# Performance work log

Measured on AMD Instinct MI355X. Metric: run time of the kernel, lower is better.

## Reference

```python
import jax, jax.numpy as jnp
import numpy as np

N, E, C, R, HID = 50000, 500000, 64, 16, 64


def setup_inputs() -> dict:
    key = jax.random.key(0)
    ks = jax.random.split(key, 24)
    g = lambda k, shape, s=1.0: jax.random.normal(k, shape, dtype=jnp.float32) * s
    cs = C ** -0.5
    inp = {
        "h": g(ks[0], (N, 4 * C)),                                  # [N, 64x0e | 64x1o]
        "edge_index": jax.random.randint(ks[1], (2, E), 0, N),       # row0 = sender, row1 = receiver
        "edge_sh": g(ks[2], (E, 4)),                                 # Y_00, Y_1m (1x0e+1x1o)
        "edge_rbf": g(ks[3], (E, R)),                                # radial embedding 16x0e
        # interaction: linear_up (per-l channel mixing)
        "W_up0": g(ks[4], (C, C), cs), "W_up1": g(ks[5], (C, C), cs),
        # radial MLP 16->64->64->64->4*C (4 uvu tensor-product paths per channel)
        "M1": g(ks[6], (R, HID), R ** -0.5), "M2": g(ks[7], (HID, HID), HID ** -0.5),
        "M3": g(ks[8], (HID, HID), HID ** -0.5), "M4": g(ks[9], (HID, 4 * C), HID ** -0.5),
        # post-scatter linear
        "W_lin0": g(ks[10], (C, C), cs), "W_lin1": g(ks[11], (C, C), cs),
        # skip tensor product with 1x0e node attrs == linear residual
        "Wsc0": g(ks[12], (C, C), cs), "Wsc1": g(ks[13], (C, C), cs),
        # symmetric contraction weights (correlation <=3): 0e paths [a, a^2, v.v, a^3, a*v.v], 1o paths [v, a*v, a^2*v, (v.v)*v]
        "Wc0": g(ks[14], (C, 5)), "Wc1": g(ks[15], (C, 4)),
        # product-basis output linear
        "WB0": g(ks[16], (C, C), cs), "WB1": g(ks[17], (C, C), cs),
        # equivariant batchnorm affine params
        "gamma0": jnp.ones((C,), jnp.float32), "beta0": jnp.zeros((C,), jnp.float32),
        "gamma1": jnp.ones((C,), jnp.float32),
    }
    return inp


def reference(h, edge_index, edge_sh, edge_rbf, W_up0, W_up1, M1, M2, M3, M4,
              W_lin0, W_lin1, Wsc0, Wsc1, Wc0, Wc1, WB0, WB1, gamma0, beta0, gamma1):
    n = h.shape[0]
    h0 = h[:, :C]                        # [N,C] scalars
    h1 = h[:, C:].reshape(n, C, 3)       # [N,C,3] vectors

    # ---- interaction: linear_up ----
    up0 = h0 @ W_up0
    up1 = jnp.einsum('ncx,cd->ndx', h1, W_up1)

    # ---- radial MLP -> per-edge tensor-product weights [E,4,C] ----
    r = jax.nn.silu(edge_rbf @ M1)
    r = jax.nn.silu(r @ M2)
    r = jax.nn.silu(r @ M3)
    tpw = (r @ M4).reshape(-1, 4, C)

    # ---- gather + channelwise (uvu) tensor product with edge sh ----
    snd, rcv = edge_index[0], edge_index[1]
    x0 = up0[snd]                        # [E,C]
    x1 = up1[snd]                        # [E,C,3]
    sh0 = edge_sh[:, 0]                  # [E]
    sh1 = edge_sh[:, 1:]                 # [E,3]
    inv3 = 1.0 / jnp.sqrt(jnp.float32(3.0))
    # paths: 0e*0e->0e, 0e*1o->1o, 1o*0e->1o, 1o*1o->0e (dot)
    m0e = tpw[:, 0] * x0 * sh0[:, None] + tpw[:, 3] * jnp.einsum('ecx,ex->ec', x1, sh1) * inv3
    m1e = (tpw[:, 1][:, :, None] * x0[:, :, None] * sh1[:, None, :]
           + tpw[:, 2][:, :, None] * x1 * sh0[:, None, None])

    # ---- scatter-sum to receivers (avg_num_neighbors = 1.0) ----
    msg0 = jax.ops.segment_sum(m0e, rcv, num_segments=n)
    msg1 = jax.ops.segment_sum(m1e, rcv, num_segments=n)

    # ---- post linear -> A features; skip connection sc ----
    A0 = msg0 @ W_lin0
    A1 = jnp.einsum('ncx,cd->ndx', msg1, W_lin1)
    sc0 = h0 @ Wsc0
    sc1 = jnp.einsum('ncx,cd->ndx', h1, Wsc1)

    # ---- product basis: symmetric contraction up to correlation 3 ----
    vv = jnp.sum(A1 * A1, -1)            # [N,C]
    B0 = (Wc0[:, 0] * A0 + Wc0[:, 1] * A0 * A0 + Wc0[:, 2] * vv
          + Wc0[:, 3] * A0 ** 3 + Wc0[:, 4] * A0 * vv)
    B1 = (Wc1[:, 0] + Wc1[:, 1] * A0 + Wc1[:, 2] * A0 * A0 + Wc1[:, 3] * vv)[..., None] * A1
    o0 = B0 @ WB0 + sc0
    o1 = jnp.einsum('ncx,cd->ndx', B1, WB1) + sc1

    # ---- equivariant batchnorm: mean/var for 0e, norm-only for 1o ----
    eps = jnp.float32(1e-5)
    mu = jnp.mean(o0, 0)
    xc = o0 - mu
    var = jnp.mean(xc * xc, 0)
    n0 = xc * jax.lax.rsqrt(var + eps) * gamma0 + beta0
    nrm1 = jnp.mean(jnp.sum(o1 * o1, -1) / 3.0, 0)
    n1 = o1 * (jax.lax.rsqrt(nrm1 + eps) * gamma1)[None, :, None]

    return jnp.concatenate([n0, n1.reshape(n, 3 * C)], -1)
```

## Files before the change

kernel.cpp:

```cpp
#include <hip/hip_runtime.h>
#include <hip/hip_fp16.h>
#include <math.h>

#define NN 50000
#define NE 500000

typedef __attribute__((ext_vector_type(8))) short bf16x8;
typedef __attribute__((ext_vector_type(4))) float f32x4;

__device__ __forceinline__ float silu_f(float x) {
  return x / (1.0f + __expf(-x));
}
__device__ __forceinline__ unsigned short f2bf(float x) {
  union { float f; unsigned u; } v;
  v.f = x;
  unsigned r = v.u + 0x7fffu + ((v.u >> 16) & 1u);
  return (unsigned short)(r >> 16);
}
__device__ __forceinline__ unsigned short f2h(float x) {
  __half h = __float2half(x);
  return *reinterpret_cast<unsigned short*>(&h);
}
__device__ __forceinline__ float h2f(unsigned short u) {
  __half h = *reinterpret_cast<__half*>(&u);
  return __half2float(h);
}
__device__ __forceinline__ void splitbf(float x, unsigned short& hi_,
                                        unsigned short& lo_) {
  unsigned short h = f2bf(x);
  union { unsigned u; float f; } v;
  v.u = (unsigned)h << 16;
  hi_ = h;
  lo_ = f2bf(x - v.f);
}
__device__ __forceinline__ int swz64(int row, int col) {
  return row * 64 + ((((col >> 3) ^ (row & 7)) << 3) | (col & 7));
}
__device__ __forceinline__ int swz32(int row, int col) {
  return row * 32 + ((((col >> 3) ^ (row & 3)) << 3) | (col & 7));
}
__device__ __forceinline__ bf16x8 wfrag(const unsigned short* Wt, int n,
                                        int kc, int q) {
  return *reinterpret_cast<const bf16x8*>(
      &Wt[n * 64 + (((kc * 4 + q) ^ (n & 7)) << 3)]);
}
__device__ __forceinline__ bf16x8 ldfrag(const float* p) {
  float4 f0 = *reinterpret_cast<const float4*>(p);
  float4 f1 = *reinterpret_cast<const float4*>(p + 4);
  bf16x8 a;
  a[0] = (short)f2bf(f0.x); a[1] = (short)f2bf(f0.y);
  a[2] = (short)f2bf(f0.z); a[3] = (short)f2bf(f0.w);
  a[4] = (short)f2bf(f1.x); a[5] = (short)f2bf(f1.y);
  a[6] = (short)f2bf(f1.z); a[7] = (short)f2bf(f1.w);
  return a;
}
__device__ __forceinline__ void ldfrag2(const float* p, bf16x8& hi,
                                        bf16x8& lo) {
  float4 f0 = *reinterpret_cast<const float4*>(p);
  float4 f1 = *reinterpret_cast<const float4*>(p + 4);
  float a[8] = {f0.x, f0.y, f0.z, f0.w, f1.x, f1.y, f1.z, f1.w};
#pragma unroll
  for (int i = 0; i < 8; ++i) {
    unsigned short h, l2;
    splitbf(a[i], h, l2);
    hi[i] = (short)h;
    lo[i] = (short)l2;
  }
}
__device__ __forceinline__ f32x4 mfma_(bf16x8 a, bf16x8 b, f32x4 cacc) {
  return __builtin_amdgcn_mfma_f32_16x16x32_bf16(a, b, cacc, 0, 0, 0);
}

__global__ __launch_bounds__(256) void ksort1(const int* __restrict__ eidx,
                                              int* __restrict__ hist) {
  int e = blockIdx.x * 256 + threadIdx.x;
  if (e < NE) atomicAdd(&hist[eidx[NE + e]], 1);
}

__global__ __launch_bounds__(1024) void ksort2(const int* __restrict__ hist,
                                               int* __restrict__ cursor) {
  __shared__ int bs[1024];
  const int t = threadIdx.x;
  const int CH = (NN + 1023) / 1024;
  const int lo = t * CH, hi = (lo + CH < NN) ? lo + CH : NN;
  int s = 0;
  for (int i = lo; i < hi; ++i) s += hist[i];
  bs[t] = s;
  __syncthreads();
  for (int off = 1; off < 1024; off <<= 1) {
    int v = (t >= off) ? bs[t - off] : 0;
    __syncthreads();
    bs[t] += v;
    __syncthreads();
  }
  int run = bs[t] - s;
  for (int i = lo; i < hi; ++i) {
    cursor[i] = run;
    run += hist[i];
  }
}

__global__ __launch_bounds__(256) void ksort3(const int* __restrict__ eidx,
                                              int* __restrict__ cursor,
                                              int* __restrict__ perm) {
  int e = blockIdx.x * 256 + threadIdx.x;
  if (e < NE) {
    int p = atomicAdd(&cursor[eidx[NE + e]], 1);
    perm[p] = e;
  }
}

__global__ __launch_bounds__(256) void kup(
    const float* __restrict__ h, const float* __restrict__ Wup0,
    const float* __restrict__ Wup1, unsigned short* __restrict__ upb) {
  __shared__ float shd[4][256];
  const int w = threadIdx.x >> 6, j = threadIdx.x & 63;
  const int n = blockIdx.x * 4 + w;
  const float* hr = h + (size_t)n * 256;
#pragma unroll
  for (int t = 0; t < 4; ++t) shd[w][t * 64 + j] = hr[t * 64 + j];
  __syncthreads();
  float a0 = 0.f, ax = 0.f, ay = 0.f, az = 0.f;
#pragma unroll 8
  for (int c = 0; c < 64; ++c) {
    float h0 = shd[w][c];
    float hx = shd[w][64 + 3 * c + 0];
    float hy = shd[w][64 + 3 * c + 1];
    float hz = shd[w][64 + 3 * c + 2];
    float w0 = Wup0[c * 64 + j];
    float w1 = Wup1[c * 64 + j];
    a0 = fmaf(h0, w0, a0);
    ax = fmaf(hx, w1, ax);
    ay = fmaf(hy, w1, ay);
    az = fmaf(hz, w1, az);
  }
  ushort4 pk;
  pk.x = f2h(a0);
  pk.y = f2h(ax);
  pk.z = f2h(ay);
  pk.w = f2h(az);
  *reinterpret_cast<ushort4*>(upb + ((size_t)n * 64 + j) * 4) = pk;
}

__global__ __launch_bounds__(512) void kedge(
    const float* __restrict__ rbf, const int* __restrict__ eidx,
    const float* __restrict__ esh, const float* __restrict__ M1,
    const float* __restrict__ M2, const float* __restrict__ M3,
    const float* __restrict__ M4, const unsigned short* __restrict__ upb,
    const int* __restrict__ perm, float* __restrict__ msg0,
    float* __restrict__ msg1) {
  __shared__ unsigned short M1t[64 * 32];
  __shared__ unsigned short M2t[64 * 64];
  __shared__ unsigned short M3t[64 * 64];
  __shared__ unsigned short M4t[256 * 64];
  __shared__ unsigned short actS[8][32 * 64];
  const int tid = threadIdx.x;
  const int w = tid >> 6, l = tid & 63;
  const int c = l & 15, q = l >> 4;

  for (int i = tid; i < 2048; i += 512) {
    int o = i >> 5, k = i & 31;
    M1t[swz32(o, k)] = (k < 16) ? f2bf(M1[k * 64 + o]) : (unsigned short)0;
  }
  for (int i = tid; i < 4096; i += 512) {
    int k = i >> 6, o = i & 63;
    M2t[swz64(o, k)] = f2bf(M2[i]);
    M3t[swz64(o, k)] = f2bf(M3[i]);
  }
  for (int i = tid; i < 16384; i += 512) {
    int k = i >> 8, o = i & 255;
    M4t[swz64(o, k)] = f2bf(M4[i]);
  }
  __syncthreads();

  unsigned short* act = actS[w];
  const float inv3 = 0.57735026918962576f;
  const int NW = NE / 32;
  const int scq = (c >> 2) * 8 + (c & 3);

  for (int grp = blockIdx.x; grp < (NW + 7) / 8; grp += gridDim.x) {
    const int gw = grp * 8 + w;
    if (gw >= NW) continue;
    const int eb = gw * 32;

#pragma unroll
    for (int t = 0; t < 2; ++t) {
      const int sc = scq + t * 4;
      bf16x8 a1 = {};
      if (q < 2) {
        const int pec = perm[eb + sc];
        const float* p = rbf + (size_t)pec * 16 + q * 8;
        float4 f0 = *reinterpret_cast<const float4*>(p);
        float4 f1 = *reinterpret_cast<const float4*>(p + 4);
        a1[0] = (short)f2bf(f0.x); a1[1] = (short)f2bf(f0.y);
        a1[2] = (short)f2bf(f0.z); a1[3] = (short)f2bf(f0.w);
        a1[4] = (short)f2bf(f1.x); a1[5] = (short)f2bf(f1.y);
        a1[6] = (short)f2bf(f1.z); a1[7] = (short)f2bf(f1.w);
      }
      f32x4 acc[4];
#pragma unroll
      for (int nt = 0; nt < 4; ++nt) {
        int n = nt * 16 + c;
        bf16x8 b = *reinterpret_cast<const bf16x8*>(&M1t[n * 32 + ((q ^ (n & 3)) << 3)]);
        f32x4 z = {0.f, 0.f, 0.f, 0.f};
        acc[nt] = __builtin_amdgcn_mfma_f32_16x16x32_bf16(a1, b, z, 0, 0, 0);
      }
#pragma unroll
      for (int nt = 0; nt < 4; ++nt)
#pragma unroll
        for (int r = 0; r < 4; ++r)
          act[swz64(q * 8 + t * 4 + r, nt * 16 + c)] = f2bf(silu_f(acc[nt][r]));

      {
        bf16x8 a0 = *reinterpret_cast<const bf16x8*>(&act[sc * 64 + (((0 + q) ^ (sc & 7)) << 3)]);
        bf16x8 a1b = *reinterpret_cast<const bf16x8*>(&act[sc * 64 + (((4 + q) ^ (sc & 7)) << 3)]);
#pragma unroll
        for (int nt = 0; nt < 4; ++nt) {
          int n = nt * 16 + c;
          f32x4 z = {0.f, 0.f, 0.f, 0.f};
          acc[nt] = __builtin_amdgcn_mfma_f32_16x16x32_bf16(a0, wfrag(M2t, n, 0, q), z, 0, 0, 0);
          acc[nt] = __builtin_amdgcn_mfma_f32_16x16x32_bf16(a1b, wfrag(M2t, n, 1, q), acc[nt], 0, 0, 0);
        }
#pragma unroll
        for (int nt = 0; nt < 4; ++nt)
#pragma unroll
          for (int r = 0; r < 4; ++r)
            act[swz64(q * 8 + t * 4 + r, nt * 16 + c)] = f2bf(silu_f(acc[nt][r]));
      }
      {
        bf16x8 a0 = *reinterpret_cast<const bf16x8*>(&act[sc * 64 + (((0 + q) ^ (sc & 7)) << 3)]);
        bf16x8 a1b = *reinterpret_cast<const bf16x8*>(&act[sc * 64 + (((4 + q) ^ (sc & 7)) << 3)]);
#pragma unroll
        for (int nt = 0; nt < 4; ++nt) {
          int n = nt * 16 + c;
          f32x4 z = {0.f, 0.f, 0.f, 0.f};
          acc[nt] = __builtin_amdgcn_mfma_f32_16x16x32_bf16(a0, wfrag(M3t, n, 0, q), z, 0, 0, 0);
          acc[nt] = __builtin_amdgcn_mfma_f32_16x16x32_bf16(a1b, wfrag(M3t, n, 1, q), acc[nt], 0, 0, 0);
        }
#pragma unroll
        for (int nt = 0; nt < 4; ++nt)
#pragma unroll
          for (int r = 0; r < 4; ++r)
            act[swz64(q * 8 + t * 4 + r, nt * 16 + c)] = f2bf(silu_f(acc[nt][r]));
      }
    }

    int sn[8], rvv[8];
    float4 shv[8];
#pragma unroll
    for (int r8 = 0; r8 < 8; ++r8) {
      const int e2 = perm[eb + 8 * q + r8];
      sn[r8] = eidx[e2];
      rvv[r8] = eidx[NE + e2];
      shv[r8] = *reinterpret_cast<const float4*>(esh + (size_t)e2 * 4);
    }
    bf16x8 a0t[2], a1t[2];
#pragma unroll
    for (int t = 0; t < 2; ++t) {
      const int sc = scq + t * 4;
      a0t[t] = *reinterpret_cast<const bf16x8*>(&act[sc * 64 + (((0 + q) ^ (sc & 7)) << 3)]);
      a1t[t] = *reinterpret_cast<const bf16x8*>(&act[sc * 64 + (((4 + q) ^ (sc & 7)) << 3)]);
    }
#pragma unroll
    for (int j2 = 0; j2 < 4; ++j2) {
      const int ch = j2 * 16 + c;
      float acc0 = 0.f, accx = 0.f, accy = 0.f, accz = 0.f;
      int cur = rvv[0];
#pragma unroll
      for (int t = 0; t < 2; ++t) {
        ushort4 xv[4];
#pragma unroll
        for (int r = 0; r < 4; ++r)
          xv[r] = *reinterpret_cast<const ushort4*>(
              upb + ((size_t)sn[4 * t + r] * 64 + ch) * 4);
        f32x4 t4[4];
#pragma unroll
        for (int m = 0; m < 4; ++m) {
          int n = (m * 4 + j2) * 16 + c;
          f32x4 z = {0.f, 0.f, 0.f, 0.f};
          t4[m] = __builtin_amdgcn_mfma_f32_16x16x32_bf16(a0t[t], wfrag(M4t, n, 0, q), z, 0, 0, 0);
          t4[m] = __builtin_amdgcn_mfma_f32_16x16x32_bf16(a1t[t], wfrag(M4t, n, 1, q), t4[m], 0, 0, 0);
        }
#pragma unroll
        for (int r = 0; r < 4; ++r) {
          const int idx = 4 * t + r;
          float x0 = h2f(xv[r].x);
          float xx = h2f(xv[r].y);
          float xy = h2f(xv[r].z);
          float xz = h2f(xv[r].w);
          float t0v = t4[0][r], t1v = t4[1][r];
          float t2v = t4[2][r], t3v = t4[3][r];
          float4 sh4 = shv[idx];
          float dot = xx * sh4.y + xy * sh4.z + xz * sh4.w;
          float m0 = t0v * x0 * sh4.x + t3v * dot * inv3;
          float a1v = t1v * x0, b1v = t2v * sh4.x;
          float m1x = fmaf(a1v, sh4.y, b1v * xx);
          float m1y = fmaf(a1v, sh4.z, b1v * xy);
          float m1z = fmaf(a1v, sh4.w, b1v * xz);
          if (rvv[idx] != cur) {
            atomicAdd(msg0 + (size_t)cur * 64 + ch, acc0);
            atomicAdd(msg1 + (size_t)cur * 192 + ch, accx);
            atomicAdd(msg1 + (size_t)cur * 192 + 64 + ch, accy);
            atomicAdd(msg1 + (size_t)cur * 192 + 128 + ch, accz);
            cur = rvv[idx];
            acc0 = accx = accy = accz = 0.f;
          }
          acc0 += m0;
          accx += m1x;
          accy += m1y;
          accz += m1z;
        }
      }
      atomicAdd(msg0 + (size_t)cur * 64 + ch, acc0);
      atomicAdd(msg1 + (size_t)cur * 192 + ch, accx);
      atomicAdd(msg1 + (size_t)cur * 192 + 64 + ch, accy);
      atomicAdd(msg1 + (size_t)cur * 192 + 128 + ch, accz);
    }
  }
}

__global__ __launch_bounds__(512) void knode(
    const float* __restrict__ msg0, const float* __restrict__ msg1,
    const float* __restrict__ h, const float* __restrict__ Wl0,
    const float* __restrict__ Wl1, const float* __restrict__ Wsc0,
    const float* __restrict__ Wsc1, const float* __restrict__ Wc0,
    const float* __restrict__ Wc1, const float* __restrict__ WB0,
    const float* __restrict__ WB1, float* __restrict__ out,
    float* __restrict__ stat) {
  extern __shared__ unsigned short klds[];
  unsigned short* actS = klds + 10 * 4096;
  const int tid = threadIdx.x, w = tid >> 6, l = tid & 63;
  const int c = l & 15, q = l >> 4;
  for (int i = tid; i < 4096; i += 512) {
    int k = i >> 6, o = i & 63;
    int s = swz64(o, k);
    unsigned short hi, lo;
    splitbf(Wl0[i], hi, lo);
    klds[s] = hi; klds[4096 + s] = lo;
    splitbf(Wl1[i], hi, lo);
    klds[2 * 4096 + s] = hi; klds[3 * 4096 + s] = lo;
    klds[4 * 4096 + s] = f2bf(Wsc0[i]);
    klds[5 * 4096 + s] = f2bf(Wsc1[i]);
    splitbf(WB0[i], hi, lo);
    klds[6 * 4096 + s] = hi; klds[7 * 4096 + s] = lo;
    splitbf(WB1[i], hi, lo);
    klds[8 * 4096 + s] = hi; klds[9 * 4096 + s] = lo;
  }
  __syncthreads();
  const int gw = blockIdx.x * 8 + w;
  const bool valid = (gw < NN / 16);
  const int gws = valid ? gw : 0;
  const int n0 = gws * 16;
  const int nc = n0 + c;
  unsigned short* actH = actS + w * 2048;
  unsigned short* actL = actH + 1024;
  const unsigned short* Wl0h = klds;
  const unsigned short* Wl0l = klds + 4096;
  const unsigned short* Wl1h = klds + 2 * 4096;
  const unsigned short* Wl1l = klds + 3 * 4096;
  const unsigned short* Wsc0t = klds + 4 * 4096;
  const unsigned short* Wsc1t = klds + 5 * 4096;
  const unsigned short* WB0h = klds + 6 * 4096;
  const unsigned short* WB0l = klds + 7 * 4096;
  const unsigned short* WB1h = klds + 8 * 4096;
  const unsigned short* WB1l = klds + 9 * 4096;

  f32x4 aA0[4], aA1[3][4];
  {
    bf16x8 h0, l0, h1, l1;
    ldfrag2(msg0 + (size_t)nc * 64 + q * 8, h0, l0);
    ldfrag2(msg0 + (size_t)nc * 64 + 32 + q * 8, h1, l1);
#pragma unroll
    for (int nt = 0; nt < 4; ++nt) {
      int n = nt * 16 + c;
      f32x4 z = {0.f, 0.f, 0.f, 0.f};
      f32x4 v = mfma_(h0, wfrag(Wl0h, n, 0, q), z);
      v = mfma_(l0, wfrag(Wl0h, n, 0, q), v);
      v = mfma_(h0, wfrag(Wl0l, n, 0, q), v);
      v = mfma_(h1, wfrag(Wl0h, n, 1, q), v);
      v = mfma_(l1, wfrag(Wl0h, n, 1, q), v);
      v = mfma_(h1, wfrag(Wl0l, n, 1, q), v);
      aA0[nt] = v;
    }
#pragma unroll
    for (int x = 0; x < 3; ++x) {
      ldfrag2(msg1 + (size_t)nc * 192 + x * 64 + q * 8, h0, l0);
      ldfrag2(msg1 + (size_t)nc * 192 + x * 64 + 32 + q * 8, h1, l1);
#pragma unroll
      for (int nt = 0; nt < 4; ++nt) {
        int n = nt * 16 + c;
        f32x4 z = {0.f, 0.f, 0.f, 0.f};
        f32x4 v = mfma_(h0, wfrag(Wl1h, n, 0, q), z);
        v = mfma_(l0, wfrag(Wl1h, n, 0, q), v);
        v = mfma_(h0, wfrag(Wl1l, n, 0, q), v);
        v = mfma_(h1, wfrag(Wl1h, n, 1, q), v);
        v = mfma_(l1, wfrag(Wl1h, n, 1, q), v);
        v = mfma_(h1, wfrag(Wl1l, n, 1, q), v);
        aA1[x][nt] = v;
      }
    }
  }
#pragma unroll
  for (int nt = 0; nt < 4; ++nt) {
    const int ch = nt * 16 + c;
    const float* wc0 = Wc0 + ch * 5;
    const float4 c1 = *reinterpret_cast<const float4*>(Wc1 + ch * 4);
#pragma unroll
    for (int r = 0; r < 4; ++r) {
      float A0v = aA0[nt][r];
      float ax = aA1[0][nt][r], ay = aA1[1][nt][r], az = aA1[2][nt][r];
      float vv = ax * ax + ay * ay + az * az;
      float A02 = A0v * A0v;
      float B0 = wc0[0] * A0v + wc0[1] * A02 + wc0[2] * vv +
                 wc0[3] * A02 * A0v + wc0[4] * A0v * vv;
      float sB = c1.x + c1.y * A0v + c1.z * A02 + c1.w * vv;
      aA0[nt][r] = B0;
      aA1[0][nt][r] = sB * ax;
      aA1[1][nt][r] = sB * ay;
      aA1[2][nt][r] = sB * az;
    }
  }
  float st0[4], sq0[4], st1[4];
#pragma unroll
  for (int nt = 0; nt < 4; ++nt) { st0[nt] = 0.f; sq0[nt] = 0.f; st1[nt] = 0.f; }
  const float* hrow = h + (size_t)nc * 256;

  {
#pragma unroll
    for (int nt = 0; nt < 4; ++nt)
#pragma unroll
      for (int r = 0; r < 4; ++r) {
        unsigned short hh, ll;
        splitbf(aA0[nt][r], hh, ll);
        int s = swz64(4 * q + r, nt * 16 + c);
        actH[s] = hh;
        actL[s] = ll;
      }
    __syncthreads();
    bf16x8 bh0 = *reinterpret_cast<const bf16x8*>(&actH[c * 64 + ((q ^ (c & 7)) << 3)]);
    bf16x8 bh1 = *reinterpret_cast<const bf16x8*>(&actH[c * 64 + (((4 + q) ^ (c & 7)) << 3)]);
    bf16x8 bl0 = *reinterpret_cast<const bf16x8*>(&actL[c * 64 + ((q ^ (c & 7)) << 3)]);
    bf16x8 bl1 = *reinterpret_cast<const bf16x8*>(&actL[c * 64 + (((4 + q) ^ (c & 7)) << 3)]);
    __syncthreads();
    bf16x8 ah0 = ldfrag(hrow + q * 8);
    bf16x8 ah1 = ldfrag(hrow + 32 + q * 8);
    f32x4 o[4];
#pragma unroll
    for (int nt = 0; nt < 4; ++nt) {
      int n = nt * 16 + c;
      f32x4 z = {0.f, 0.f, 0.f, 0.f};
      f32x4 v = mfma_(ah0, wfrag(Wsc0t, n, 0, q), z);
      v = mfma_(ah1, wfrag(Wsc0t, n, 1, q), v);
      v = mfma_(bh0, wfrag(WB0h, n, 0, q), v);
      v = mfma_(bh1, wfrag(WB0h, n, 1, q), v);
      v = mfma_(bl0, wfrag(WB0h, n, 0, q), v);
      v = mfma_(bl1, wfrag(WB0h, n, 1, q), v);
      v = mfma_(bh0, wfrag(WB0l, n, 0, q), v);
      v = mfma_(bh1, wfrag(WB0l, n, 1, q), v);
      o[nt] = v;
    }
    if (valid) {
#pragma unroll
      for (int nt = 0; nt < 4; ++nt) {
        const int ch = nt * 16 + c;
#pragma unroll
        for (int r = 0; r < 4; ++r) {
          float v = o[nt][r];
          out[(size_t)(n0 + 4 * q + r) * 256 + ch] = v;
          st0[nt] += v;
          sq0[nt] = fmaf(v, v, sq0[nt]);
        }
      }
    }
  }
#pragma unroll
  for (int x = 0; x < 3; ++x) {
#pragma unroll
    for (int nt = 0; nt < 4; ++nt)
#pragma unroll
      for (int r = 0; r < 4; ++r) {
        unsigned short hh, ll;
        splitbf(aA1[x][nt][r], hh, ll);
        int s = swz64(4 * q + r, nt * 16 + c);
        actH[s] = hh;
        actL[s] = ll;
      }
    __syncthreads();
    bf16x8 bh0 = *reinterpret_cast<const bf16x8*>(&actH[c * 64 + ((q ^ (c & 7)) << 3)]);
    bf16x8 bh1 = *reinterpret_cast<const bf16x8*>(&actH[c * 64 + (((4 + q) ^ (c & 7)) << 3)]);
    bf16x8 bl0 = *reinterpret_cast<const bf16x8*>(&actL[c * 64 + ((q ^ (c & 7)) << 3)]);
    bf16x8 bl1 = *reinterpret_cast<const bf16x8*>(&actL[c * 64 + (((4 + q) ^ (c & 7)) << 3)]);
    __syncthreads();
    bf16x8 ah0, ah1;
#pragma unroll
    for (int i = 0; i < 8; ++i) {
      ah0[i] = (short)f2bf(hrow[64 + (q * 8 + i) * 3 + x]);
      ah1[i] = (short)f2bf(hrow[64 + (32 + q * 8 + i) * 3 + x]);
    }
    f32x4 o[4];
#pragma unroll
    for (int nt = 0; nt < 4; ++nt) {
      int n = nt * 16 + c;
      f32x4 z = {0.f, 0.f, 0.f, 0.f};
      f32x4 v = mfma_(ah0, wfrag(Wsc1t, n, 0, q), z);
      v = mfma_(ah1, wfrag(Wsc1t, n, 1, q), v);
      v = mfma_(bh0, wfrag(WB1h, n, 0, q), v);
      v = mfma_(bh1, wfrag(WB1h, n, 1, q), v);
      v = mfma_(bl0, wfrag(WB1h, n, 0, q), v);
      v = mfma_(bl1, wfrag(WB1h, n, 1, q), v);
      v = mfma_(bh0, wfrag(WB1l, n, 0, q), v);
      v = mfma_(bh1, wfrag(WB1l, n, 1, q), v);
      o[nt] = v;
    }
    if (valid) {
#pragma unroll
      for (int nt = 0; nt < 4; ++nt) {
        const int ch = nt * 16 + c;
#pragma unroll
        for (int r = 0; r < 4; ++r) {
          float v = o[nt][r];
          out[(size_t)(n0 + 4 * q + r) * 256 + 64 + 3 * ch + x] = v;
          st1[nt] = fmaf(v, v, st1[nt]);
        }
      }
    }
  }
  if (valid) {
#pragma unroll
    for (int nt = 0; nt < 4; ++nt) {
      float v0 = st0[nt], v1 = sq0[nt], v2 = st1[nt];
      v0 += __shfl_xor(v0, 16); v0 += __shfl_xor(v0, 32);
      v1 += __shfl_xor(v1, 16); v1 += __shfl_xor(v1, 32);
      v2 += __shfl_xor(v2, 16); v2 += __shfl_xor(v2, 32);
      if (q == 0) {
        atomicAdd(stat + nt * 16 + c, v0);
        atomicAdd(stat + 64 + nt * 16 + c, v1);
        atomicAdd(stat + 128 + nt * 16 + c, v2);
      }
    }
  }
}

__global__ void kstat(const float* __restrict__ stat_in,
                      float* __restrict__ stat_out,
                      const float* __restrict__ gamma0,
                      const float* __restrict__ gamma1) {
  const int j = threadIdx.x;
  const float invN = 1.0f / (float)NN;
  float mu = stat_in[j] * invN;
  float var = stat_in[64 + j] * invN - mu * mu;
  float s0 = rsqrtf(var + 1e-5f) * gamma0[j];
  float nr = stat_in[128 + j] * (invN / 3.0f);
  float s1 = rsqrtf(nr + 1e-5f) * gamma1[j];
  stat_out[j] = mu;
  stat_out[64 + j] = s0;
  stat_out[128 + j] = s1;
}

__global__ __launch_bounds__(256) void knorm(float* __restrict__ out,
                                             const float* __restrict__ stat,
                                             const float* __restrict__ beta0) {
  const int w = threadIdx.x >> 6, j = threadIdx.x & 63;
  const int n = blockIdx.x * 4 + w;
  const float mu = stat[192 + j], s0 = stat[256 + j], s1 = stat[320 + j];
  const float b0 = beta0[j];
  float* orow = out + (size_t)n * 256;
  orow[j] = (orow[j] - mu) * s0 + b0;
#pragma unroll
  for (int x = 0; x < 3; ++x) orow[64 + 3 * j + x] *= s1;
}

extern "C" void kernel_launch(void* const* d_in, const int* in_sizes, int n_in,
                              void* d_out, int out_size, void* d_ws,
                              size_t ws_size, hipStream_t stream) {
  (void)in_sizes; (void)n_in; (void)out_size; (void)ws_size;
  const float* h = (const float*)d_in[0];
  const int* eidx = (const int*)d_in[1];
  const float* esh = (const float*)d_in[2];
  const float* erbf = (const float*)d_in[3];
  const float* Wup0 = (const float*)d_in[4];
  const float* Wup1 = (const float*)d_in[5];
  const float* M1 = (const float*)d_in[6];
  const float* M2 = (const float*)d_in[7];
  const float* M3 = (const float*)d_in[8];
  const float* M4 = (const float*)d_in[9];
  const float* Wl0 = (const float*)d_in[10];
  const float* Wl1 = (const float*)d_in[11];
  const float* Wsc0 = (const float*)d_in[12];
  const float* Wsc1 = (const float*)d_in[13];
  const float* Wc0 = (const float*)d_in[14];
  const float* Wc1 = (const float*)d_in[15];
  const float* WB0 = (const float*)d_in[16];
  const float* WB1 = (const float*)d_in[17];
  const float* gamma0 = (const float*)d_in[18];
  const float* beta0 = (const float*)d_in[19];
  const float* gamma1 = (const float*)d_in[20];

  float* ws = (float*)d_ws;
  unsigned short* upb = (unsigned short*)ws;
  float* msg0 = ws + (size_t)NN * 256;
  float* msg1 = ws + (size_t)NN * 320;
  float* stat = ws + (size_t)NN * 512;
  float* outf = (float*)d_out;

  int* hist = (int*)d_out;
  int* cursor = hist + NN;
  int* perm = cursor + NN;

  hipMemsetAsync(msg0, 0, ((size_t)NN * 256 + 384) * sizeof(float), stream);
  hipMemsetAsync(hist, 0, (size_t)NN * sizeof(int), stream);

  hipFuncSetAttribute((const void*)knode,
                      hipFuncAttributeMaxDynamicSharedMemorySize, 114688);

  const int EG = (NE + 255) / 256;
  ksort1<<<EG, 256, 0, stream>>>(eidx, hist);
  ksort2<<<1, 1024, 0, stream>>>(hist, cursor);
  ksort3<<<EG, 256, 0, stream>>>(eidx, cursor, perm);
  kup<<<NN / 4, 256, 0, stream>>>(h, Wup0, Wup1, upb);
  kedge<<<512, 512, 0, stream>>>(erbf, eidx, esh, M1, M2, M3, M4, upb, perm,
                                 msg0, msg1);
  knode<<<(NN / 16 + 7) / 8, 512, 114688, stream>>>(
      msg0, msg1, h, Wl0, Wl1, Wsc0, Wsc1, Wc0, Wc1, WB0, WB1, outf, stat);
  kstat<<<1, 64, 0, stream>>>(stat, stat + 192, gamma0, gamma1);
  knorm<<<NN / 4, 256, 0, stream>>>(outf, stat, beta0);
}
```

Before: 487.1 us.

## Process 64-edge tiles per wave in kedge with LDS-staged edge metadata

Each wave in the edge kernel now handles 64 sorted edges per iteration instead of 32. The radial MLP runs over four 16-row sub-tiles, reusing a smaller per-wave LDS activation buffer guarded by explicit lgkmcnt waits. Sender, receiver and spherical-harmonic data are loaded once per lane into LDS and read back per row. Each lane's segmented reduction now spans 16 consecutive edges instead of 8, which is meant to cut atomic flushes and per-edge index loads. The cost is more register pressure, extra LDS traffic, and tail handling for partial tiles.

```diff
diff --git a/kernel.cpp b/kernel.cpp
--- a/kernel.cpp
+++ b/kernel.cpp
@@ -69,6 +69,9 @@
 }
 __device__ __forceinline__ f32x4 mfma_(bf16x8 a, bf16x8 b, f32x4 cacc) {
   return __builtin_amdgcn_mfma_f32_16x16x32_bf16(a, b, cacc, 0, 0, 0);
+}
+__device__ __forceinline__ void lds_fence() {
+  asm volatile("s_waitcnt lgkmcnt(0)" ::: "memory");
 }
 
 __global__ __launch_bounds__(256) void ksort1(const int* __restrict__ eidx,
@@ -153,7 +156,7 @@
   __shared__ unsigned short M2t[64 * 64];
   __shared__ unsigned short M3t[64 * 64];
   __shared__ unsigned short M4t[256 * 64];
-  __shared__ unsigned short actS[8][32 * 64];
+  __shared__ float actF[8][512];
   const int tid = threadIdx.x;
   const int w = tid >> 6, l = tid & 63;
   const int c = l & 15, q = l >> 4;
@@ -173,29 +176,31 @@
   }
   __syncthreads();
 
-  unsigned short* act = actS[w];
+  unsigned short* act = (unsigned short*)actF[w];
+  float* msh = actF[w];
+  int* msn = (int*)(actF[w] + 256);
+  int* mrv = (int*)(actF[w] + 320);
   const float inv3 = 0.57735026918962576f;
-  const int NW = NE / 32;
-  const int scq = (c >> 2) * 8 + (c & 3);
-
-  for (int grp = blockIdx.x; grp < (NW + 7) / 8; grp += gridDim.x) {
-    const int gw = grp * 8 + w;
-    if (gw >= NW) continue;
-    const int eb = gw * 32;
-
-#pragma unroll
-    for (int t = 0; t < 2; ++t) {
-      const int sc = scq + t * 4;
-      bf16x8 a1 = {};
+  const int NG = (NE + 63) >> 6;
+  const int srow = (c >> 2) * 16 + (c & 3);
+
+  for (int g = blockIdx.x * 8 + w; g < NG; g += gridDim.x * 8) {
+    const int eb = g * 64;
+    const int ecnt = min(64, NE - eb);
+    bf16x8 a0t[4], a1t[4];
+#pragma unroll
+    for (int t = 0; t < 4; ++t) {
+      bf16x8 a1v = {};
       if (q < 2) {
-        const int pec = perm[eb + sc];
+        const int sr = min(srow + t * 4, ecnt - 1);
+        const int pec = perm[eb + sr];
         const float* p = rbf + (size_t)pec * 16 + q * 8;
         float4 f0 = *reinterpret_cast<const float4*>(p);
         float4 f1 = *reinterpret_cast<const float4*>(p + 4);
-        a1[0] = (short)f2bf(f0.x); a1[1] = (short)f2bf(f0.y);
-        a1[2] = (short)f2bf(f0.z); a1[3] = (short)f2bf(f0.w);
-        a1[4] = (short)f2bf(f1.x); a1[5] = (short)f2bf(f1.y);
-        a1[6] = (short)f2bf(f1.z); a1[7] = (short)f2bf(f1.w);
+        a1v[0] = (short)f2bf(f0.x); a1v[1] = (short)f2bf(f0.y);
+        a1v[2] = (short)f2bf(f0.z); a1v[3] = (short)f2bf(f0.w);
+        a1v[4] = (short)f2bf(f1.x); a1v[5] = (short)f2bf(f1.y);
+        a1v[6] = (short)f2bf(f1.z); a1v[7] = (short)f2bf(f1.w);
       }
       f32x4 acc[4];
 #pragma unroll
@@ -203,17 +208,17 @@
         int n = nt * 16 + c;
         bf16x8 b = *reinterpret_cast<const bf16x8*>(&M1t[n * 32 + ((q ^ (n & 3)) << 3)]);
         f32x4 z = {0.f, 0.f, 0.f, 0.f};
-        acc[nt] = __builtin_amdgcn_mfma_f32_16x16x32_bf16(a1, b, z, 0, 0, 0);
+        acc[nt] = __builtin_amdgcn_mfma_f32_16x16x32_bf16(a1v, b, z, 0, 0, 0);
       }
 #pragma unroll
       for (int nt = 0; nt < 4; ++nt)
 #pragma unroll
         for (int r = 0; r < 4; ++r)
-          act[swz64(q * 8 + t * 4 + r, nt * 16 + c)] = f2bf(silu_f(acc[nt][r]));
-
+          act[swz64(4 * q + r, nt * 16 + c)] = f2bf(silu_f(acc[nt][r]));
+      lds_fence();
       {
-        bf16x8 a0 = *reinterpret_cast<const bf16x8*>(&act[sc * 64 + (((0 + q) ^ (sc & 7)) << 3)]);
-        bf16x8 a1b = *reinterpret_cast<const bf16x8*>(&act[sc * 64 + (((4 + q) ^ (sc & 7)) << 3)]);
+        bf16x8 a0 = *reinterpret_cast<const bf16x8*>(&act[c * 64 + ((q ^ (c & 7)) << 3)]);
+        bf16x8 a1b = *reinterpret_cast<const bf16x8*>(&act[c * 64 + (((4 + q) ^ (c & 7)) << 3)]);
 #pragma unroll
         for (int nt = 0; nt < 4; ++nt) {
           int n = nt * 16 + c;
@@ -221,15 +226,17 @@
           acc[nt] = __builtin_amdgcn_mfma_f32_16x16x32_bf16(a0, wfrag(M2t, n, 0, q), z, 0, 0, 0);
           acc[nt] = __builtin_amdgcn_mfma_f32_16x16x32_bf16(a1b, wfrag(M2t, n, 1, q), acc[nt], 0, 0, 0);
         }
+        lds_fence();
 #pragma unroll
         for (int nt = 0; nt < 4; ++nt)
 #pragma unroll
           for (int r = 0; r < 4; ++r)
-            act[swz64(q * 8 + t * 4 + r, nt * 16 + c)] = f2bf(silu_f(acc[nt][r]));
+            act[swz64(4 * q + r, nt * 16 + c)] = f2bf(silu_f(acc[nt][r]));
+        lds_fence();
       }
       {
-        bf16x8 a0 = *reinterpret_cast<const bf16x8*>(&act[sc * 64 + (((0 + q) ^ (sc & 7)) << 3)]);
-        bf16x8 a1b = *reinterpret_cast<const bf16x8*>(&act[sc * 64 + (((4 + q) ^ (sc & 7)) << 3)]);
+        bf16x8 a0 = *reinterpret_cast<const bf16x8*>(&act[c * 64 + ((q ^ (c & 7)) << 3)]);
+        bf16x8 a1b = *reinterpret_cast<const bf16x8*>(&act[c * 64 + (((4 + q) ^ (c & 7)) << 3)]);
 #pragma unroll
         for (int nt = 0; nt < 4; ++nt) {
           int n = nt * 16 + c;
@@ -237,42 +244,48 @@
           acc[nt] = __builtin_amdgcn_mfma_f32_16x16x32_bf16(a0, wfrag(M3t, n, 0, q), z, 0, 0, 0);
           acc[nt] = __builtin_amdgcn_mfma_f32_16x16x32_bf16(a1b, wfrag(M3t, n, 1, q), acc[nt], 0, 0, 0);
         }
+        lds_fence();
 #pragma unroll
         for (int nt = 0; nt < 4; ++nt)
 #pragma unroll
           for (int r = 0; r < 4; ++r)
-            act[swz64(q * 8 + t * 4 + r, nt * 16 + c)] = f2bf(silu_f(acc[nt][r]));
-      }
-    }
-
-    int sn[8], rvv[8];
-    float4 shv[8];
-#pragma unroll
-    for (int r8 = 0; r8 < 8; ++r8) {
-      const int e2 = perm[eb + 8 * q + r8];
-      sn[r8] = eidx[e2];
-      rvv[r8] = eidx[NE + e2];
-      shv[r8] = *reinterpret_cast<const float4*>(esh + (size_t)e2 * 4);
-    }
-    bf16x8 a0t[2], a1t[2];
-#pragma unroll
-    for (int t = 0; t < 2; ++t) {
-      const int sc = scq + t * 4;
-      a0t[t] = *reinterpret_cast<const bf16x8*>(&act[sc * 64 + (((0 + q) ^ (sc & 7)) << 3)]);
-      a1t[t] = *reinterpret_cast<const bf16x8*>(&act[sc * 64 + (((4 + q) ^ (sc & 7)) << 3)]);
+            act[swz64(4 * q + r, nt * 16 + c)] = f2bf(silu_f(acc[nt][r]));
+        lds_fence();
+      }
+      a0t[t] = *reinterpret_cast<const bf16x8*>(&act[c * 64 + ((q ^ (c & 7)) << 3)]);
+      a1t[t] = *reinterpret_cast<const bf16x8*>(&act[c * 64 + (((4 + q) ^ (c & 7)) << 3)]);
+      lds_fence();
+    }
+    {
+      const int sl = min(l, ecnt - 1);
+      const int e2 = perm[eb + sl];
+      msn[l] = eidx[e2];
+      mrv[l] = eidx[NE + e2];
+      *reinterpret_cast<float4*>(&msh[l * 4]) =
+          *reinterpret_cast<const float4*>(esh + (size_t)e2 * 4);
+      lds_fence();
     }
 #pragma unroll
     for (int j2 = 0; j2 < 4; ++j2) {
       const int ch = j2 * 16 + c;
       float acc0 = 0.f, accx = 0.f, accy = 0.f, accz = 0.f;
-      int cur = rvv[0];
-#pragma unroll
-      for (int t = 0; t < 2; ++t) {
+      int cur = -1;
+#pragma unroll
+      for (int t = 0; t < 4; ++t) {
+        int sn4[4], rv4[4];
+        float4 sh4v[4];
+#pragma unroll
+        for (int r = 0; r < 4; ++r) {
+          const int s = 16 * q + 4 * t + r;
+          sn4[r] = msn[s];
+          rv4[r] = mrv[s];
+          sh4v[r] = *reinterpret_cast<const float4*>(&msh[s * 4]);
+        }
         ushort4 xv[4];
 #pragma unroll
         for (int r = 0; r < 4; ++r)
           xv[r] = *reinterpret_cast<const ushort4*>(
-              upb + ((size_t)sn[4 * t + r] * 64 + ch) * 4);
+              upb + ((size_t)sn4[r] * 64 + ch) * 4);
         f32x4 t4[4];
 #pragma unroll
         for (int m = 0; m < 4; ++m) {
@@ -283,26 +296,29 @@
         }
 #pragma unroll
         for (int r = 0; r < 4; ++r) {
-          const int idx = 4 * t + r;
+          const int s = 16 * q + 4 * t + r;
+          if (s >= ecnt) continue;
           float x0 = h2f(xv[r].x);
           float xx = h2f(xv[r].y);
           float xy = h2f(xv[r].z);
           float xz = h2f(xv[r].w);
           float t0v = t4[0][r], t1v = t4[1][r];
           float t2v = t4[2][r], t3v = t4[3][r];
-          float4 sh4 = shv[idx];
+          float4 sh4 = sh4v[r];
           float dot = xx * sh4.y + xy * sh4.z + xz * sh4.w;
           float m0 = t0v * x0 * sh4.x + t3v * dot * inv3;
-          float a1v = t1v * x0, b1v = t2v * sh4.x;
-          float m1x = fmaf(a1v, sh4.y, b1v * xx);
-          float m1y = fmaf(a1v, sh4.z, b1v * xy);
-          float m1z = fmaf(a1v, sh4.w, b1v * xz);
-          if (rvv[idx] != cur) {
-            atomicAdd(msg0 + (size_t)cur * 64 + ch, acc0);
-            atomicAdd(msg1 + (size_t)cur * 192 + ch, accx);
-            atomicAdd(msg1 + (size_t)cur * 192 + 64 + ch, accy);
-            atomicAdd(msg1 + (size_t)cur * 192 + 128 + ch, accz);
-            cur = rvv[idx];
+          float a1m = t1v * x0, b1m = t2v * sh4.x;
+          float m1x = fmaf(a1m, sh4.y, b1m * xx);
+          float m1y = fmaf(a1m, sh4.z, b1m * xy);
+          float m1z = fmaf(a1m, sh4.w, b1m * xz);
+          if (rv4[r] != cur) {
+            if (cur >= 0) {
+              atomicAdd(msg0 + (size_t)cur * 64 + ch, acc0);
+              atomicAdd(msg1 + (size_t)cur * 192 + ch, accx);
+              atomicAdd(msg1 + (size_t)cur * 192 + 64 + ch, accy);
+              atomicAdd(msg1 + (size_t)cur * 192 + 128 + ch, accz);
+            }
+            cur = rv4[r];
             acc0 = accx = accy = accz = 0.f;
           }
           acc0 += m0;
@@ -311,10 +327,12 @@
           accz += m1z;
         }
       }
-      atomicAdd(msg0 + (size_t)cur * 64 + ch, acc0);
-      atomicAdd(msg1 + (size_t)cur * 192 + ch, accx);
-      atomicAdd(msg1 + (size_t)cur * 192 + 64 + ch, accy);
-      atomicAdd(msg1 + (size_t)cur * 192 + 128 + ch, accz);
+      if (cur >= 0) {
+        atomicAdd(msg0 + (size_t)cur * 64 + ch, acc0);
+        atomicAdd(msg1 + (size_t)cur * 192 + ch, accx);
+        atomicAdd(msg1 + (size_t)cur * 192 + 64 + ch, accy);
+        atomicAdd(msg1 + (size_t)cur * 192 + 128 + ch, accz);
+      }
     }
   }
 }
```

After: 526.1 us. 1.08x slower.
